# Performance work log

Hardware: AMD Instinct MI355X
Metric: run time of the kernel (lower is better)

## Reference

```python
import jax, jax.numpy as jnp
import numpy as np
from jax import lax

B, C, H, W = 8, 32, 256, 512
MAXDISP = 48


def setup_inputs() -> dict:
    key = jax.random.key(0)
    k1, k2 = jax.random.split(key)
    x = jax.random.normal(k1, (B, C, H, W), dtype=jnp.float32)
    y = jax.random.normal(k2, (B, C, H, W), dtype=jnp.float32)
    return {"x": x, "y": y, "maxdisp": MAXDISP}


def reference(x, y, maxdisp):
    # cost[:, d, :, w] = mean_c( x[:, :, :, w] * y[:, :, :, w-d] ) for w >= d, else 0
    width = x.shape[-1]
    col = jnp.arange(width)

    def step(_, d):
        # roll y right by d along width; wrapped columns are masked out below
        y_shift = jnp.roll(y, d, axis=-1)              # [B,C,H,W]
        c = jnp.mean(x * y_shift, axis=1)              # [B,H,W]
        c = jnp.where(col >= d, c, jnp.float32(0))     # zero invalid (wrapped) cols
        return None, c

    _, cost = lax.scan(step, None, jnp.arange(maxdisp))  # [D,B,H,W]
    return jnp.transpose(cost, (1, 0, 2, 3))             # [B,D,H,W]
```

## Files before the change

### kernel.cpp

```cpp
#include <hip/hip_runtime.h>


constexpr int kB = 8;
constexpr int kC = 32;
constexpr int kH = 256;
constexpr int kW = 512;
constexpr int kD = 48;

constexpr int WT = 128;
constexpr int YW = kD + WT;
constexpr int NT = 192;

__global__ __launch_bounds__(NT) void corr_kernel(
    const float* __restrict__ x, const float* __restrict__ y, float* __restrict__ out)
{
    __shared__ __align__(16) float xs[kC][WT];
    __shared__ __align__(16) float ys[kC][YW];

    const int tid = threadIdx.x;
    const int w0 = blockIdx.x * WT;
    const int h  = blockIdx.y;
    const int b  = blockIdx.z;

    const size_t chan_stride = (size_t)kH * kW;
    const float* xb = x + ((size_t)b * kC * kH + h) * kW + w0;
    const float* yb = y + ((size_t)b * kC * kH + h) * kW + (w0 - kD);

    #pragma unroll 2
    for (int idx = tid; idx < kC * (WT / 4); idx += NT) {
        int c   = idx >> 5;
        int col = (idx & 31) << 2;
        float4 v = *(const float4*)(xb + (size_t)c * chan_stride + col);
        *(float4*)&xs[c][col] = v;
    }
    #pragma unroll 2
    for (int idx = tid; idx < kC * (YW / 4); idx += NT) {
        int c   = idx / (YW / 4);
        int col = (idx % (YW / 4)) << 2;
        float4 v;
        if (w0 - kD + col >= 0) {
            v = *(const float4*)(yb + (size_t)c * chan_stride + col);
        } else {
            v = make_float4(0.f, 0.f, 0.f, 0.f);
        }
        *(float4*)&ys[c][col] = v;
    }
    __syncthreads();

    const int wg  = tid & 15;
    const int dg  = tid >> 4;
    const int wi  = wg << 3;
    const int db  = dg << 2;
    const int yb0 = wi + (kD - 4) - db;

    float acc[4][8];
    #pragma unroll
    for (int dd = 0; dd < 4; ++dd)
        #pragma unroll
        for (int j = 0; j < 8; ++j) acc[dd][j] = 0.f;

    #pragma unroll 4
    for (int c = 0; c < kC; ++c) {
        float4 x0 = *(const float4*)&xs[c][wi];
        float4 x1 = *(const float4*)&xs[c][wi + 4];
        float4 y0 = *(const float4*)&ys[c][yb0];
        float4 y1 = *(const float4*)&ys[c][yb0 + 4];
        float4 y2 = *(const float4*)&ys[c][yb0 + 8];
        float xv[8]  = {x0.x, x0.y, x0.z, x0.w, x1.x, x1.y, x1.z, x1.w};
        float yv[12] = {y0.x, y0.y, y0.z, y0.w, y1.x, y1.y, y1.z, y1.w,
                        y2.x, y2.y, y2.z, y2.w};
        #pragma unroll
        for (int dd = 0; dd < 4; ++dd)
            #pragma unroll
            for (int j = 0; j < 8; ++j)
                acc[dd][j] += xv[j] * yv[4 - dd + j];
    }

    const float scale = 1.0f / kC;
    #pragma unroll
    for (int dd = 0; dd < 4; ++dd) {
        int d = db + dd;
        float* o = out + (((size_t)b * kD + d) * kH + h) * kW + w0 + wi;
        float4 o0 = make_float4(acc[dd][0] * scale, acc[dd][1] * scale,
                                acc[dd][2] * scale, acc[dd][3] * scale);
        float4 o1 = make_float4(acc[dd][4] * scale, acc[dd][5] * scale,
                                acc[dd][6] * scale, acc[dd][7] * scale);
        *(float4*)(o)     = o0;
        *(float4*)(o + 4) = o1;
    }
}

extern "C" void kernel_launch(void* const* d_in, const int* in_sizes, int n_in,
                              void* d_out, int out_size, void* d_ws, size_t ws_size,
                              hipStream_t stream) {
    const float* x = (const float*)d_in[0];
    const float* y = (const float*)d_in[1];
    float* out = (float*)d_out;

    dim3 grid(kW / WT, kH, kB);
    corr_kernel<<<grid, NT, 0, stream>>>(x, y, out);
}
```

Baseline: 454.5 us.

## Retile correlation per thread to 12 disparities by 4 columns, stage channels in halves

Each thread now computes 12 disparities for 4 adjacent columns instead of 4 disparities for 8 columns, using 128 threads per block. The channel dimension is staged through shared memory in two halves of 16, which halves the LDS footprint and should allow more resident blocks. The intent is to raise FMA work per shared-memory load and improve occupancy. The cost is an extra barrier between halves and a larger accumulator array per thread, which adds register pressure.

Result: faster. 410.8 us (-9.6%).

```diff
diff --git a/kernel.cpp b/kernel.cpp
--- a/kernel.cpp
+++ b/kernel.cpp
@@ -9,84 +9,83 @@
 
 constexpr int WT = 128;
 constexpr int YW = kD + WT;
-constexpr int NT = 192;
+constexpr int NT = 128;
+constexpr int CH = 16;
+constexpr int DP = 12;
+constexpr int WP = 4;
 
 __global__ __launch_bounds__(NT) void corr_kernel(
     const float* __restrict__ x, const float* __restrict__ y, float* __restrict__ out)
 {
-    __shared__ __align__(16) float xs[kC][WT];
-    __shared__ __align__(16) float ys[kC][YW];
+    __shared__ __align__(16) float xs[CH][WT];
+    __shared__ __align__(16) float ys[CH][YW];
 
     const int tid = threadIdx.x;
-    const int w0 = blockIdx.x * WT;
-    const int h  = blockIdx.y;
-    const int b  = blockIdx.z;
+    const int w0  = blockIdx.x * WT;
+    const int h   = blockIdx.y;
+    const int b   = blockIdx.z;
 
-    const size_t chan_stride = (size_t)kH * kW;
+    const size_t cs = (size_t)kH * kW;
     const float* xb = x + ((size_t)b * kC * kH + h) * kW + w0;
     const float* yb = y + ((size_t)b * kC * kH + h) * kW + (w0 - kD);
 
-    #pragma unroll 2
-    for (int idx = tid; idx < kC * (WT / 4); idx += NT) {
-        int c   = idx >> 5;
-        int col = (idx & 31) << 2;
-        float4 v = *(const float4*)(xb + (size_t)c * chan_stride + col);
-        *(float4*)&xs[c][col] = v;
-    }
-    #pragma unroll 2
-    for (int idx = tid; idx < kC * (YW / 4); idx += NT) {
-        int c   = idx / (YW / 4);
-        int col = (idx % (YW / 4)) << 2;
-        float4 v;
-        if (w0 - kD + col >= 0) {
-            v = *(const float4*)(yb + (size_t)c * chan_stride + col);
-        } else {
-            v = make_float4(0.f, 0.f, 0.f, 0.f);
+    const int lw    = tid & 31;
+    const int dgrp  = tid >> 5;
+    const int wi    = lw << 2;
+    const int d0    = dgrp * DP;
+    const int ybase = wi + 36 - d0;
+
+    float acc[DP][WP];
+    #pragma unroll
+    for (int dd = 0; dd < DP; ++dd)
+        #pragma unroll
+        for (int j = 0; j < WP; ++j) acc[dd][j] = 0.f;
+
+    for (int p = 0; p < 2; ++p) {
+        if (p) __syncthreads();
+
+        #pragma unroll
+        for (int idx = tid; idx < CH * (WT / 4); idx += NT) {
+            int c   = idx >> 5;
+            int col = (idx & 31) << 2;
+            *(float4*)&xs[c][col] =
+                *(const float4*)(xb + (size_t)(p * CH + c) * cs + col);
         }
-        *(float4*)&ys[c][col] = v;
-    }
-    __syncthreads();
+        #pragma unroll
+        for (int idx = tid; idx < CH * (YW / 4); idx += NT) {
+            int c   = idx / (YW / 4);
+            int col = (idx % (YW / 4)) << 2;
+            float4 v = make_float4(0.f, 0.f, 0.f, 0.f);
+            if (w0 - kD + col >= 0)
+                v = *(const float4*)(yb + (size_t)(p * CH + c) * cs + col);
+            *(float4*)&ys[c][col] = v;
+        }
+        __syncthreads();
 
-    const int wg  = tid & 15;
-    const int dg  = tid >> 4;
-    const int wi  = wg << 3;
-    const int db  = dg << 2;
-    const int yb0 = wi + (kD - 4) - db;
-
-    float acc[4][8];
-    #pragma unroll
-    for (int dd = 0; dd < 4; ++dd)
-        #pragma unroll
-        for (int j = 0; j < 8; ++j) acc[dd][j] = 0.f;
-
-    #pragma unroll 4
-    for (int c = 0; c < kC; ++c) {
-        float4 x0 = *(const float4*)&xs[c][wi];
-        float4 x1 = *(const float4*)&xs[c][wi + 4];
-        float4 y0 = *(const float4*)&ys[c][yb0];
-        float4 y1 = *(const float4*)&ys[c][yb0 + 4];
-        float4 y2 = *(const float4*)&ys[c][yb0 + 8];
-        float xv[8]  = {x0.x, x0.y, x0.z, x0.w, x1.x, x1.y, x1.z, x1.w};
-        float yv[12] = {y0.x, y0.y, y0.z, y0.w, y1.x, y1.y, y1.z, y1.w,
-                        y2.x, y2.y, y2.z, y2.w};
-        #pragma unroll
-        for (int dd = 0; dd < 4; ++dd)
+        #pragma unroll 4
+        for (int c = 0; c < CH; ++c) {
+            float4 x4 = *(const float4*)&xs[c][wi];
+            float4 y0 = *(const float4*)&ys[c][ybase];
+            float4 y1 = *(const float4*)&ys[c][ybase + 4];
+            float4 y2 = *(const float4*)&ys[c][ybase + 8];
+            float4 y3 = *(const float4*)&ys[c][ybase + 12];
+            float xv[4]  = {x4.x, x4.y, x4.z, x4.w};
+            float yv[16] = {y0.x, y0.y, y0.z, y0.w, y1.x, y1.y, y1.z, y1.w,
+                            y2.x, y2.y, y2.z, y2.w, y3.x, y3.y, y3.z, y3.w};
             #pragma unroll
-            for (int j = 0; j < 8; ++j)
-                acc[dd][j] += xv[j] * yv[4 - dd + j];
+            for (int dd = 0; dd < DP; ++dd)
+                #pragma unroll
+                for (int j = 0; j < WP; ++j)
+                    acc[dd][j] += xv[j] * yv[j + 12 - dd];
+        }
     }
 
     const float scale = 1.0f / kC;
     #pragma unroll
-    for (int dd = 0; dd < 4; ++dd) {
-        int d = db + dd;
-        float* o = out + (((size_t)b * kD + d) * kH + h) * kW + w0 + wi;
-        float4 o0 = make_float4(acc[dd][0] * scale, acc[dd][1] * scale,
-                                acc[dd][2] * scale, acc[dd][3] * scale);
-        float4 o1 = make_float4(acc[dd][4] * scale, acc[dd][5] * scale,
-                                acc[dd][6] * scale, acc[dd][7] * scale);
-        *(float4*)(o)     = o0;
-        *(float4*)(o + 4) = o1;
+    for (int dd = 0; dd < DP; ++dd) {
+        float* o = out + (((size_t)b * kD + d0 + dd) * kH + h) * kW + w0 + wi;
+        *(float4*)o = make_float4(acc[dd][0] * scale, acc[dd][1] * scale,
+                                  acc[dd][2] * scale, acc[dd][3] * scale);
     }
 }
 
```
